# Optimization experiments

Hardware: AMD Instinct MI355X
Metric: run time of the kernel (lower is better)

Reference implementation:

```python
import jax, jax.numpy as jnp
import numpy as np

B, T, D = 1, 1024, 1024
H, KVH, HD = 16, 4, 64          # heads, kv heads, head dim (D = H*HD)
E, K, FF = 8, 2, 2048           # experts, top_k, expert hidden
CF, ROPE_THETA, CLIP = 2.0, 500000.0, 8.0
CAP = int(np.ceil(B * T * K * CF / E))  # per-expert capacity (=512)
EPS = 1e-5


def layernorm(x, w):
    mu = jnp.mean(x, -1, keepdims=True)
    var = jnp.var(x, -1, keepdims=True)
    return (x - mu) * jax.lax.rsqrt(var + EPS) * w


def rotate_half(u):
    u1, u2 = u[..., : HD // 2], u[..., HD // 2 :]
    return jnp.concatenate([-u2, u1], axis=-1)


def rope(q, k, position_ids):
    inv_freq = 1.0 / (ROPE_THETA ** (jnp.arange(0, HD, 2, dtype=jnp.float32) / HD))
    ang = position_ids.astype(jnp.float32)[..., None] * inv_freq  # (B,T,HD/2)
    emb = jnp.concatenate([ang, ang], axis=-1)                    # (B,T,HD)
    cos = jnp.cos(emb)[:, :, None, :]  # broadcast over heads -> (B,T,1,HD)
    sin = jnp.sin(emb)[:, :, None, :]
    q = q * cos + rotate_half(q) * sin
    k = k * cos + rotate_half(k) * sin
    return q, k


def setup_inputs() -> dict:
    key = jax.random.key(0)
    ks = jax.random.split(key, 12)
    s = 0.02
    return {
        "hidden_states": jax.random.normal(ks[0], (B, T, D), jnp.float32),
        "position_ids": jnp.tile(jnp.arange(T, dtype=jnp.int32)[None, :], (B, 1)),
        "ln1_w": jnp.ones((D,), jnp.float32),
        "ln2_w": jnp.ones((D,), jnp.float32),
        "Wq": jax.random.normal(ks[1], (D, H * HD), jnp.float32) * s,
        "Wk": jax.random.normal(ks[2], (D, KVH * HD), jnp.float32) * s,
        "Wv": jax.random.normal(ks[3], (D, KVH * HD), jnp.float32) * s,
        "Wo": jax.random.normal(ks[4], (H * HD, D), jnp.float32) * s,
        "Wr": jax.random.normal(ks[5], (D, E), jnp.float32) * s,
        "Wg": jax.random.normal(ks[6], (E, D, FF), jnp.float32) * s,
        "Wu": jax.random.normal(ks[7], (E, D, FF), jnp.float32) * s,
        "Wd": jax.random.normal(ks[8], (E, FF, D), jnp.float32) * s,
    }


def reference(hidden_states, position_ids, ln1_w, ln2_w, Wq, Wk, Wv, Wo, Wr, Wg, Wu, Wd):
    x = hidden_states
    # ---- attention (pre-LN, clip_qkv, RoPE, GQA, causal) ----
    res = x
    h = layernorm(x, ln1_w)
    q = jnp.clip(h @ Wq, -CLIP, CLIP).reshape(B, T, H, HD)
    k = jnp.clip(h @ Wk, -CLIP, CLIP).reshape(B, T, KVH, HD)
    v = jnp.clip(h @ Wv, -CLIP, CLIP).reshape(B, T, KVH, HD)
    q, k = rope(q, k, position_ids)
    k = jnp.repeat(k, H // KVH, axis=2)  # GQA expand -> (B,T,H,HD)
    v = jnp.repeat(v, H // KVH, axis=2)
    scores = jnp.einsum("bthd,bshd->bhts", q, k) / jnp.sqrt(jnp.float32(HD))
    causal = jnp.tril(jnp.ones((T, T), bool))
    scores = jnp.where(causal[None, None], scores, jnp.finfo(scores.dtype).min)
    attn = jax.nn.softmax(scores, axis=-1)
    o = jnp.einsum("bhts,bshd->bthd", attn, v).reshape(B, T, H * HD) @ Wo
    x = res + o
    # ---- MoE FFN (top-k router, capacity-based dispatch, GLU experts) ----
    res = x
    h = layernorm(x, ln2_w).reshape(B * T, D)
    N = B * T
    probs = jax.nn.softmax(h @ Wr, axis=-1)            # (N,E)
    vals, idx = jax.lax.top_k(probs, K)                # (N,K)
    gate = vals / jnp.sum(vals, -1, keepdims=True)     # normalize_top_k_affinities
    e_flat = idx.reshape(-1)                           # (N*K,)
    g_flat = gate.reshape(-1)
    tok = jnp.repeat(jnp.arange(N), K)                 # source token per assignment
    oh = jax.nn.one_hot(e_flat, E, dtype=jnp.int32)
    pos = jnp.cumsum(oh, axis=0)[jnp.arange(N * K), e_flat] - 1  # slot within expert
    keep = pos < CAP                                   # capacity drop mask
    slot = jnp.where(keep, pos, CAP)                   # overflow -> trash slot
    xb = jnp.zeros((E, CAP + 1, D), h.dtype).at[e_flat, slot].set(h[tok])
    act = jax.nn.silu(jnp.einsum("ecd,edf->ecf", xb, Wg)) * jnp.einsum("ecd,edf->ecf", xb, Wu)
    ob = jnp.einsum("ecf,efd->ecd", act, Wd)           # (E,CAP+1,D)
    contrib = ob[e_flat, slot] * (g_flat * keep.astype(h.dtype))[:, None]
    y = jnp.zeros((N, D), h.dtype).at[tok].add(contrib).reshape(B, T, D)
    return res + y
```

## Files before the change

### kernel.cpp

```cpp
#include <hip/hip_runtime.h>
#include <math.h>

typedef __attribute__((ext_vector_type(8))) short bfrag;
typedef __attribute__((ext_vector_type(8))) unsigned short u16x8;
typedef __attribute__((ext_vector_type(4))) float f32x4;

__device__ __forceinline__ unsigned short bf16_rne(float f) {
  unsigned int u = __float_as_uint(f);
  u += 0x7FFFu + ((u >> 16) & 1u);
  return (unsigned short)(u >> 16);
}
__device__ __forceinline__ float bf16f(unsigned short h) {
  return __uint_as_float(((unsigned int)h) << 16);
}
__device__ __forceinline__ void split3(float x, unsigned short &o1, unsigned short &o2, unsigned short &o3) {
  o1 = bf16_rne(x);
  const float r1 = x - bf16f(o1);
  o2 = bf16_rne(r1);
  const float r2 = r1 - bf16f(o2);
  o3 = bf16_rne(r2);
}
__device__ __forceinline__ void split2(float x, unsigned short &o1, unsigned short &o2) {
  o1 = bf16_rne(x);
  o2 = bf16_rne(x - bf16f(o1));
}

__global__ __launch_bounds__(256) void ln_kernel(const float* __restrict__ x,
                                                 const float* __restrict__ w,
                                                 float* __restrict__ out) {
  const int t = blockIdx.x;
  const int tid = threadIdx.x;
  const float4 v = *reinterpret_cast<const float4*>(&x[(size_t)t * 1024 + tid * 4]);
  float s = v.x + v.y + v.z + v.w;
  float ss = v.x * v.x + v.y * v.y + v.z * v.z + v.w * v.w;
#pragma unroll
  for (int off = 32; off; off >>= 1) {
    s += __shfl_xor(s, off);
    ss += __shfl_xor(ss, off);
  }
  __shared__ float red1[4], red2[4];
  if ((tid & 63) == 0) { red1[tid >> 6] = s; red2[tid >> 6] = ss; }
  __syncthreads();
  s = red1[0] + red1[1] + red1[2] + red1[3];
  ss = red2[0] + red2[1] + red2[2] + red2[3];
  const float mu = s * (1.0f / 1024.0f);
  const float var = ss * (1.0f / 1024.0f) - mu * mu;
  const float rstd = 1.0f / sqrtf(var + 1e-5f);
  const float4 wv = *reinterpret_cast<const float4*>(&w[tid * 4]);
  float4 o;
  o.x = (v.x - mu) * rstd * wv.x;
  o.y = (v.y - mu) * rstd * wv.y;
  o.z = (v.z - mu) * rstd * wv.z;
  o.w = (v.w - mu) * rstd * wv.w;
  *reinterpret_cast<float4*>(&out[(size_t)t * 1024 + tid * 4]) = o;
}

__global__ __launch_bounds__(256) void split3_conv_kernel(
    const float* __restrict__ src, unsigned short* __restrict__ d1,
    unsigned short* __restrict__ d2, unsigned short* __restrict__ d3) {
  const int i = blockIdx.x * 256 + threadIdx.x;
  const float4 v = reinterpret_cast<const float4*>(src)[i];
  ushort4 a, b, c;
  split3(v.x, a.x, b.x, c.x);
  split3(v.y, a.y, b.y, c.y);
  split3(v.z, a.z, b.z, c.z);
  split3(v.w, a.w, b.w, c.w);
  reinterpret_cast<ushort4*>(d1)[i] = a;
  reinterpret_cast<ushort4*>(d2)[i] = b;
  reinterpret_cast<ushort4*>(d3)[i] = c;
}

__global__ __launch_bounds__(256) void split3t_kernel(
    const float* __restrict__ src, unsigned short* __restrict__ d1,
    unsigned short* __restrict__ d2, unsigned short* __restrict__ d3,
    int K, int N) {
  __shared__ float tile[32][33];
  const int k0 = blockIdx.x * 32, n0 = blockIdx.y * 32;
  const int tx = threadIdx.x & 31, ty = threadIdx.x >> 5;
#pragma unroll
  for (int i = 0; i < 4; ++i)
    tile[ty + i * 8][tx] = src[(size_t)(k0 + ty + i * 8) * N + n0 + tx];
  __syncthreads();
#pragma unroll
  for (int i = 0; i < 4; ++i) {
    const float v = tile[tx][ty + i * 8];
    unsigned short s1, s2, s3;
    split3(v, s1, s2, s3);
    const size_t o = (size_t)(n0 + ty + i * 8) * K + k0 + tx;
    d1[o] = s1; d2[o] = s2; d3[o] = s3;
  }
}

__global__ __launch_bounds__(256) void gemm_ps_kernel(
    const unsigned short* __restrict__ A1, const unsigned short* __restrict__ A2,
    const unsigned short* __restrict__ A3, const unsigned short* __restrict__ B1,
    const unsigned short* __restrict__ B2, const unsigned short* __restrict__ B3,
    float* __restrict__ C, const float* __restrict__ Res,
    int N, int K, int doclip) {
  __shared__ alignas(16) unsigned short As[3][32][40];
  __shared__ alignas(16) unsigned short Bs[3][64][40];
  const int tid = threadIdx.x;
  const int m0 = blockIdx.x * 32;
  const int n0 = blockIdx.y * 64;
  const int w = tid >> 6, l = tid & 63;
  const int wm = (w & 1) * 16, wn = (w >> 1) * 32;
  const int lr = l & 15, lg = l >> 4;
  const int arow = tid >> 3, aslot = tid & 7;

  const unsigned short* Ap[3] = {A1, A2, A3};
  const unsigned short* Bp[3] = {B1, B2, B3};

  f32x4 acc[2] = {{0.f,0.f,0.f,0.f},{0.f,0.f,0.f,0.f}};

  for (int k0 = 0; k0 < K; k0 += 32) {
#pragma unroll
    for (int s = 0; s < 3; ++s) {
      *reinterpret_cast<ushort4*>(&As[s][arow][aslot * 4]) =
          *reinterpret_cast<const ushort4*>(&Ap[s][(size_t)(m0 + arow) * K + k0 + aslot * 4]);
#pragma unroll
      for (int p = 0; p < 2; ++p) {
        const int row = arow + p * 32;
        *reinterpret_cast<ushort4*>(&Bs[s][row][aslot * 4]) =
            *reinterpret_cast<const ushort4*>(&Bp[s][(size_t)(n0 + row) * K + k0 + aslot * 4]);
      }
    }
    __syncthreads();
    bfrag af[3], bg[2][3];
#pragma unroll
    for (int s = 0; s < 3; ++s)
      af[s] = *reinterpret_cast<const bfrag*>(&As[s][wm + lr][lg * 8]);
#pragma unroll
    for (int ni = 0; ni < 2; ++ni)
#pragma unroll
      for (int s = 0; s < 3; ++s)
        bg[ni][s] = *reinterpret_cast<const bfrag*>(&Bs[s][wn + ni * 16 + lr][lg * 8]);
#pragma unroll
    for (int ni = 0; ni < 2; ++ni) {
      f32x4 c = acc[ni];
      c = __builtin_amdgcn_mfma_f32_16x16x32_bf16(af[2], bg[ni][0], c, 0, 0, 0);
      c = __builtin_amdgcn_mfma_f32_16x16x32_bf16(af[1], bg[ni][1], c, 0, 0, 0);
      c = __builtin_amdgcn_mfma_f32_16x16x32_bf16(af[0], bg[ni][2], c, 0, 0, 0);
      c = __builtin_amdgcn_mfma_f32_16x16x32_bf16(af[1], bg[ni][0], c, 0, 0, 0);
      c = __builtin_amdgcn_mfma_f32_16x16x32_bf16(af[0], bg[ni][1], c, 0, 0, 0);
      c = __builtin_amdgcn_mfma_f32_16x16x32_bf16(af[0], bg[ni][0], c, 0, 0, 0);
      acc[ni] = c;
    }
    __syncthreads();
  }
#pragma unroll
  for (int ni = 0; ni < 2; ++ni)
#pragma unroll
    for (int r = 0; r < 4; ++r) {
      const int row = m0 + wm + lg * 4 + r;
      const int col = n0 + wn + ni * 16 + lr;
      float vv = acc[ni][r];
      if (doclip) vv = fminf(fmaxf(vv, -8.0f), 8.0f);
      if (Res) vv += Res[(size_t)row * N + col];
      C[(size_t)row * N + col] = vv;
    }
}

__global__ void rope_table_kernel(const int* __restrict__ posids,
                                  float* __restrict__ cosT, float* __restrict__ sinT) {
  const int t = blockIdx.x * 8 + (threadIdx.x >> 5);
  const int i = threadIdx.x & 31;
  const double ang = (double)posids[t] * pow(500000.0, -(double)i / 32.0);
  cosT[t * 32 + i] = (float)cos(ang);
  sinT[t * 32 + i] = (float)sin(ang);
}

__global__ void rope_kernel(float* __restrict__ q, float* __restrict__ k,
                            const float* __restrict__ cosT, const float* __restrict__ sinT) {
  const int t = blockIdx.x;
  const int hh = blockIdx.y;
  const int i = threadIdx.x;
  float* ptr = (hh < 16) ? &q[((size_t)t * 16 + hh) * 64]
                         : &k[((size_t)t * 4 + (hh - 16)) * 64];
  const float c = cosT[t * 32 + i], s = sinT[t * 32 + i];
  const float u1 = ptr[i], u2 = ptr[i + 32];
  ptr[i]      = u1 * c - u2 * s;
  ptr[i + 32] = u2 * c + u1 * s;
}

__global__ __launch_bounds__(256) void prep_kv_kernel(
    const float* __restrict__ k, const float* __restrict__ v,
    unsigned short* __restrict__ Kp1, unsigned short* __restrict__ Kp2,
    unsigned short* __restrict__ Vp1, unsigned short* __restrict__ Vp2) {
  const int key = blockIdx.x;
  const int kvh = threadIdx.x >> 6;
  const int d = threadIdx.x & 63;
  const float kk = k[((size_t)key * 4 + kvh) * 64 + d];
  const float vv = v[((size_t)key * 4 + kvh) * 64 + d];
  unsigned short a1, a2, b1, b2;
  split2(kk, a1, a2);
  split2(vv, b1, b2);
  const size_t ki = ((size_t)kvh * 1024 + key) * 64 + d;
  Kp1[ki] = a1; Kp2[ki] = a2;
  const size_t vi = ((size_t)kvh * 64 + d) * 1024 + key;
  Vp1[vi] = b1; Vp2[vi] = b2;
}

__global__ __launch_bounds__(256) void attn_kernel(
    const float* __restrict__ q,
    const unsigned short* __restrict__ Kp1, const unsigned short* __restrict__ Kp2,
    const unsigned short* __restrict__ Vp1, const unsigned short* __restrict__ Vp2,
    float* __restrict__ o) {
  const int qt = blockIdx.x, h = blockIdx.y, kvh = h >> 2;
  __shared__ unsigned short Ks1[64][72], Ks2[64][72], Vt1[64][72], Vt2[64][72];
  __shared__ unsigned short Ps1[4][16][72], Ps2[4][16][72];
  const int tid = threadIdx.x;
  const int w = tid >> 6, l = tid & 63;
  const int lr = l & 15, lg = l >> 4;

  bfrag aq1[2], aq2[2];
  {
    const int tq = qt * 64 + w * 16 + lr;
    const float* qrow = &q[((size_t)tq * 16 + h) * 64];
#pragma unroll
    for (int ks = 0; ks < 2; ++ks) {
      const int d0 = ks * 32 + lg * 8;
      const float4 f0 = *reinterpret_cast<const float4*>(qrow + d0);
      const float4 f1 = *reinterpret_cast<const float4*>(qrow + d0 + 4);
      const float xv[8] = {f0.x, f0.y, f0.z, f0.w, f1.x, f1.y, f1.z, f1.w};
#pragma unroll
      for (int j = 0; j < 8; ++j) {
        const float xs = xv[j] * 0.125f;
        unsigned short p1, p2;
        split2(xs, p1, p2);
        aq1[ks][j] = (short)p1;
        aq2[ks][j] = (short)p2;
      }
    }
  }

  f32x4 accO[4] = {{0.f,0.f,0.f,0.f},{0.f,0.f,0.f,0.f},{0.f,0.f,0.f,0.f},{0.f,0.f,0.f,0.f}};
  float mrun[4] = {-INFINITY, -INFINITY, -INFINITY, -INFINITY};
  float lrun[4] = {0.f, 0.f, 0.f, 0.f};

  for (int ti = 0; ti <= qt; ++ti) {
    const int s0 = ti * 64;
    {
      const size_t kbase = ((size_t)kvh * 1024 + s0 + l) * 64 + w * 16;
      *reinterpret_cast<u16x8*>(&Ks1[l][w * 16])     = *reinterpret_cast<const u16x8*>(&Kp1[kbase]);
      *reinterpret_cast<u16x8*>(&Ks1[l][w * 16 + 8]) = *reinterpret_cast<const u16x8*>(&Kp1[kbase + 8]);
      *reinterpret_cast<u16x8*>(&Ks2[l][w * 16])     = *reinterpret_cast<const u16x8*>(&Kp2[kbase]);
      *reinterpret_cast<u16x8*>(&Ks2[l][w * 16 + 8]) = *reinterpret_cast<const u16x8*>(&Kp2[kbase + 8]);
      const size_t vbase = ((size_t)kvh * 64 + l) * 1024 + s0 + w * 16;
      *reinterpret_cast<u16x8*>(&Vt1[l][w * 16])     = *reinterpret_cast<const u16x8*>(&Vp1[vbase]);
      *reinterpret_cast<u16x8*>(&Vt1[l][w * 16 + 8]) = *reinterpret_cast<const u16x8*>(&Vp1[vbase + 8]);
      *reinterpret_cast<u16x8*>(&Vt2[l][w * 16])     = *reinterpret_cast<const u16x8*>(&Vp2[vbase]);
      *reinterpret_cast<u16x8*>(&Vt2[l][w * 16 + 8]) = *reinterpret_cast<const u16x8*>(&Vp2[vbase + 8]);
    }
    __syncthreads();

    f32x4 accS[4] = {{0.f,0.f,0.f,0.f},{0.f,0.f,0.f,0.f},{0.f,0.f,0.f,0.f},{0.f,0.f,0.f,0.f}};
#pragma unroll
    for (int ks = 0; ks < 2; ++ks) {
      const int koff = ks * 32 + lg * 8;
#pragma unroll
      for (int ni = 0; ni < 4; ++ni) {
        const bfrag b1 = *reinterpret_cast<const bfrag*>(&Ks1[ni * 16 + lr][koff]);
        const bfrag b2 = *reinterpret_cast<const bfrag*>(&Ks2[ni * 16 + lr][koff]);
        f32x4 c = accS[ni];
        c = __builtin_amdgcn_mfma_f32_16x16x32_bf16(aq1[ks], b2, c, 0, 0, 0);
        c = __builtin_amdgcn_mfma_f32_16x16x32_bf16(aq2[ks], b1, c, 0, 0, 0);
        c = __builtin_amdgcn_mfma_f32_16x16x32_bf16(aq1[ks], b1, c, 0, 0, 0);
        accS[ni] = c;
      }
    }
    if (ti == qt) {
      const int rowb = w * 16 + lg * 4;
#pragma unroll
      for (int ni = 0; ni < 4; ++ni)
#pragma unroll
        for (int r = 0; r < 4; ++r)
          if (ni * 16 + lr > rowb + r) accS[ni][r] = -INFINITY;
    }
    float alpha[4];
#pragma unroll
    for (int r = 0; r < 4; ++r) {
      float tm = fmaxf(fmaxf(accS[0][r], accS[1][r]), fmaxf(accS[2][r], accS[3][r]));
      tm = fmaxf(tm, __shfl_xor(tm, 1));
      tm = fmaxf(tm, __shfl_xor(tm, 2));
      tm = fmaxf(tm, __shfl_xor(tm, 4));
      tm = fmaxf(tm, __shfl_xor(tm, 8));
      const float mnew = fmaxf(mrun[r], tm);
      alpha[r] = __expf(mrun[r] - mnew);
      mrun[r] = mnew;
      float ps = 0.f;
#pragma unroll
      for (int ni = 0; ni < 4; ++ni) {
        const float pv = __expf(accS[ni][r] - mnew);
        accS[ni][r] = pv;
        ps += pv;
      }
      ps += __shfl_xor(ps, 1);
      ps += __shfl_xor(ps, 2);
      ps += __shfl_xor(ps, 4);
      ps += __shfl_xor(ps, 8);
      lrun[r] = lrun[r] * alpha[r] + ps;
    }
#pragma unroll
    for (int ni = 0; ni < 4; ++ni)
#pragma unroll
      for (int r = 0; r < 4; ++r) {
        const float pv = accS[ni][r];
        unsigned short p1, p2;
        split2(pv, p1, p2);
        Ps1[w][lg * 4 + r][ni * 16 + lr] = p1;
        Ps2[w][lg * 4 + r][ni * 16 + lr] = p2;
      }
#pragma unroll
    for (int ni = 0; ni < 4; ++ni)
#pragma unroll
      for (int r = 0; r < 4; ++r) accO[ni][r] *= alpha[r];

    asm volatile("s_waitcnt lgkmcnt(0)" ::: "memory");

#pragma unroll
    for (int kk = 0; kk < 2; ++kk) {
      const int koff = kk * 32 + lg * 8;
      const bfrag pa1 = *reinterpret_cast<const bfrag*>(&Ps1[w][lr][koff]);
      const bfrag pa2 = *reinterpret_cast<const bfrag*>(&Ps2[w][lr][koff]);
#pragma unroll
      for (int ni = 0; ni < 4; ++ni) {
        const bfrag vb1 = *reinterpret_cast<const bfrag*>(&Vt1[ni * 16 + lr][koff]);
        const bfrag vb2 = *reinterpret_cast<const bfrag*>(&Vt2[ni * 16 + lr][koff]);
        f32x4 c = accO[ni];
        c = __builtin_amdgcn_mfma_f32_16x16x32_bf16(pa1, vb2, c, 0, 0, 0);
        c = __builtin_amdgcn_mfma_f32_16x16x32_bf16(pa2, vb1, c, 0, 0, 0);
        c = __builtin_amdgcn_mfma_f32_16x16x32_bf16(pa1, vb1, c, 0, 0, 0);
        accO[ni] = c;
      }
    }
    __syncthreads();
  }

  const int tqo = qt * 64 + w * 16 + lg * 4;
#pragma unroll
  for (int r = 0; r < 4; ++r) {
    const float inv = 1.0f / lrun[r];
#pragma unroll
    for (int ni = 0; ni < 4; ++ni)
      o[((size_t)(tqo + r) * 16 + h) * 64 + ni * 16 + lr] = accO[ni][r] * inv;
  }
}

__global__ __launch_bounds__(64) void router_kernel(const float* __restrict__ h2,
                                                    const float* __restrict__ Wr,
                                                    int* __restrict__ eidx,
                                                    float* __restrict__ egate) {
  const int t = blockIdx.x;
  const int l = threadIdx.x;
  float p[8];
#pragma unroll
  for (int e = 0; e < 8; ++e) p[e] = 0.f;
  for (int d = l; d < 1024; d += 64) {
    const float x = h2[(size_t)t * 1024 + d];
    const float4 w0 = *reinterpret_cast<const float4*>(&Wr[d * 8]);
    const float4 w1 = *reinterpret_cast<const float4*>(&Wr[d * 8 + 4]);
    p[0] += x * w0.x; p[1] += x * w0.y; p[2] += x * w0.z; p[3] += x * w0.w;
    p[4] += x * w1.x; p[5] += x * w1.y; p[6] += x * w1.z; p[7] += x * w1.w;
  }
#pragma unroll
  for (int off = 32; off; off >>= 1) {
#pragma unroll
    for (int e = 0; e < 8; ++e) p[e] += __shfl_xor(p[e], off);
  }
  if (l == 0) {
    int i0 = 0; float b0 = p[0];
#pragma unroll
    for (int e = 1; e < 8; ++e) if (p[e] > b0) { b0 = p[e]; i0 = e; }
    int i1 = -1; float b1 = -INFINITY;
#pragma unroll
    for (int e = 0; e < 8; ++e) if (e != i0 && p[e] > b1) { b1 = p[e]; i1 = e; }
    const float ex = expf(b1 - b0);
    eidx[t * 2] = i0; eidx[t * 2 + 1] = i1;
    egate[t * 2] = 1.0f / (1.0f + ex);
    egate[t * 2 + 1] = ex / (1.0f + ex);
  }
}

__global__ __launch_bounds__(256) void dispatch_kernel(
    const int* __restrict__ eidx, int* __restrict__ cnt,
    int* __restrict__ slot_token, int* __restrict__ entry_slot) {
  __shared__ unsigned char ef[2048];
  __shared__ unsigned short ch[256][8];
  const int tid = threadIdx.x;
  for (int i = tid; i < 2048; i += 256) ef[i] = (unsigned char)eidx[i];
  __syncthreads();
  int loc[8];
#pragma unroll
  for (int e = 0; e < 8; ++e) loc[e] = 0;
  const int base = tid * 8;
  for (int j = 0; j < 8; ++j) {
    const int ee = ef[base + j];
#pragma unroll
    for (int e = 0; e < 8; ++e) loc[e] += (ee == e);
  }
#pragma unroll
  for (int e = 0; e < 8; ++e) ch[tid][e] = (unsigned short)loc[e];
  __syncthreads();
  int pre[8];
#pragma unroll
  for (int e = 0; e < 8; ++e) pre[e] = 0;
  for (int t2 = 0; t2 < tid; ++t2) {
#pragma unroll
    for (int e = 0; e < 8; ++e) pre[e] += ch[t2][e];
  }
  if (tid == 255) {
#pragma unroll
    for (int e = 0; e < 8; ++e) cnt[e] = min(pre[e] + loc[e], 512);
  }
  for (int j = 0; j < 8; ++j) {
    const int i = base + j;
    const int ee = ef[i];
    int slot = 0;
#pragma unroll
    for (int e = 0; e < 8; ++e) {
      if (e == ee) { slot = pre[e]; pre[e] = pre[e] + 1; }
    }
    if (slot < 512) {
      slot_token[ee * 512 + slot] = i >> 1;
      entry_slot[i] = slot;
    } else {
      entry_slot[i] = -1;
    }
  }
}

__global__ __launch_bounds__(256) void moe_xbf_kernel(
    const float* __restrict__ h2, const int* __restrict__ cnt,
    const int* __restrict__ slot_token, unsigned short* __restrict__ xbf) {
  const int row = blockIdx.x;
  const int e = row >> 9, slot = row & 511;
  const int tid = threadIdx.x;
  ushort4 o;
  if (slot < cnt[e]) {
    const int tok = slot_token[row];
    const float4 f = *reinterpret_cast<const float4*>(&h2[(size_t)tok * 1024 + tid * 4]);
    o = make_ushort4(bf16_rne(f.x), bf16_rne(f.y), bf16_rne(f.z), bf16_rne(f.w));
  } else {
    o = make_ushort4(0, 0, 0, 0);
  }
  *reinterpret_cast<ushort4*>(&xbf[(size_t)row * 1024 + tid * 4]) = o;
}

__global__ __launch_bounds__(256, 2) void moe_mlp1_kernel(
    const unsigned short* __restrict__ xbf, const float* __restrict__ Wg,
    const float* __restrict__ Wu, const int* __restrict__ cnt,
    unsigned short* __restrict__ act) {
  const int bx = blockIdx.x;
  const int e = bx & 7, nt = bx >> 3;
  const int n0 = nt * 32;
  const int ce = cnt[e];
  if (ce <= 0) return;
  __shared__ alignas(16) unsigned short BgL[2][32][72], BuL[2][32][72];
  const int tid = threadIdx.x;
  const int w = tid >> 6, l = tid & 63;
  const int lr = l & 15, lg = l >> 4;
  const int wc = tid & 31, kq8 = tid >> 5;
  const float* WgE = Wg + (size_t)e * 1024 * 2048 + (size_t)kq8 * 8 * 2048 + n0 + wc;
  const float* WuE = Wu + (size_t)e * 1024 * 2048 + (size_t)kq8 * 8 * 2048 + n0 + wc;
  const unsigned short* xbE = xbf + (size_t)e * 512 * 1024;

  f32x4 accG[8][2], accU[8][2];
#pragma unroll
  for (int mi = 0; mi < 8; ++mi)
#pragma unroll
    for (int ni = 0; ni < 2; ++ni) {
      accG[mi][ni] = (f32x4){0.f, 0.f, 0.f, 0.f};
      accU[mi][ni] = (f32x4){0.f, 0.f, 0.f, 0.f};
    }

  float wgr[8], wur[8];
#pragma unroll
  for (int j = 0; j < 8; ++j) { wgr[j] = WgE[(size_t)j * 2048]; wur[j] = WuE[(size_t)j * 2048]; }
  {
    u16x8 g8, u8;
#pragma unroll
    for (int j = 0; j < 8; ++j) { g8[j] = bf16_rne(wgr[j]); u8[j] = bf16_rne(wur[j]); }
    *reinterpret_cast<u16x8*>(&BgL[0][wc][kq8 * 8]) = g8;
    *reinterpret_cast<u16x8*>(&BuL[0][wc][kq8 * 8]) = u8;
  }
#pragma unroll
  for (int j = 0; j < 8; ++j) { wgr[j] = WgE[(size_t)(64 + j) * 2048]; wur[j] = WuE[(size_t)(64 + j) * 2048]; }
  __syncthreads();

  for (int t = 0; t < 16; ++t) {
    const int cur = t & 1;
    bfrag bgf[2][2], buf2[2][2];
#pragma unroll
    for (int ni = 0; ni < 2; ++ni)
#pragma unroll
      for (int kf = 0; kf < 2; ++kf) {
        bgf[ni][kf]  = *reinterpret_cast<const bfrag*>(&BgL[cur][ni * 16 + lr][kf * 32 + lg * 8]);
        buf2[ni][kf] = *reinterpret_cast<const bfrag*>(&BuL[cur][ni * 16 + lr][kf * 32 + lg * 8]);
      }
    u16x8 g8, u8;
    if (t < 15) {
#pragma unroll
      for (int j = 0; j < 8; ++j) { g8[j] = bf16_rne(wgr[j]); u8[j] = bf16_rne(wur[j]); }
    }
    if (t < 14) {
      const size_t kb = (size_t)(t + 2) * 64;
#pragma unroll
      for (int j = 0; j < 8; ++j) { wgr[j] = WgE[(kb + j) * 2048]; wur[j] = WuE[(kb + j) * 2048]; }
    }
    const int kA = t * 64 + lg * 8;
#pragma unroll
    for (int mi = 0; mi < 8; ++mi) {
      const int row0 = (mi * 4 + w) * 16;
      if (row0 < ce) {
        const unsigned short* ap = &xbE[(size_t)(row0 + lr) * 1024 + kA];
        const bfrag a0 = *reinterpret_cast<const bfrag*>(ap);
        const bfrag a1 = *reinterpret_cast<const bfrag*>(ap + 32);
#pragma unroll
        for (int ni = 0; ni < 2; ++ni) {
          accG[mi][ni] = __builtin_amdgcn_mfma_f32_16x16x32_bf16(a0, bgf[ni][0], accG[mi][ni], 0, 0, 0);
          accG[mi][ni] = __builtin_amdgcn_mfma_f32_16x16x32_bf16(a1, bgf[ni][1], accG[mi][ni], 0, 0, 0);
          accU[mi][ni] = __builtin_amdgcn_mfma_f32_16x16x32_bf16(a0, buf2[ni][0], accU[mi][ni], 0, 0, 0);
          accU[mi][ni] = __builtin_amdgcn_mfma_f32_16x16x32_bf16(a1, buf2[ni][1], accU[mi][ni], 0, 0, 0);
        }
      }
    }
    if (t < 15) {
      *reinterpret_cast<u16x8*>(&BgL[cur ^ 1][wc][kq8 * 8]) = g8;
      *reinterpret_cast<u16x8*>(&BuL[cur ^ 1][wc][kq8 * 8]) = u8;
    }
    __syncthreads();
  }
#pragma unroll
  for (int mi = 0; mi < 8; ++mi) {
    const int row0 = (mi * 4 + w) * 16;
    if (row0 < ce) {
#pragma unroll
      for (int r = 0; r < 4; ++r) {
        const int m = row0 + lg * 4 + r;
        if (m < ce) {
#pragma unroll
          for (int ni = 0; ni < 2; ++ni) {
            const float gg = accG[mi][ni][r];
            const float uu = accU[mi][ni][r];
            const float a = gg / (1.0f + __expf(-gg)) * uu;
            act[((size_t)e * 512 + m) * 2048 + n0 + ni * 16 + lr] = bf16_rne(a);
          }
        }
      }
    }
  }
}

__global__ __launch_bounds__(256, 2) void moe_mlp2_kernel(
    const unsigned short* __restrict__ act, const float* __restrict__ Wd,
    const int* __restrict__ cnt, float* __restrict__ ob) {
  const int bx = blockIdx.x;
  const int e = bx & 7;
  const int rr = bx >> 3;
  const int nt = rr & 31, kc = rr >> 5;
  const int n0 = nt * 32;
  const int ce = cnt[e];
  if (ce <= 0) return;
  __shared__ alignas(16) unsigned short BsL[2][32][72];
  const int tid = threadIdx.x;
  const int w = tid >> 6, l = tid & 63;
  const int lr = l & 15, lg = l >> 4;
  const int wc = tid & 31, kq8 = tid >> 5;
  const unsigned short* actE = act + (size_t)e * 512 * 2048 + (size_t)kc * 1024;
  const float* WdE = Wd + (size_t)e * 2048 * 1024 + (size_t)(kc * 1024 + kq8 * 8) * 1024 + n0 + wc;
  float* obE = ob + (size_t)kc * 8 * 512 * 1024;

  f32x4 acc[8][2];
#pragma unroll
  for (int mi = 0; mi < 8; ++mi)
#pragma unroll
    for (int ni = 0; ni < 2; ++ni) acc[mi][ni] = (f32x4){0.f, 0.f, 0.f, 0.f};

  float wdr[8];
#pragma unroll
  for (int j = 0; j < 8; ++j) wdr[j] = WdE[(size_t)j * 1024];
  {
    u16x8 d8;
#pragma unroll
    for (int j = 0; j < 8; ++j) d8[j] = bf16_rne(wdr[j]);
    *reinterpret_cast<u16x8*>(&BsL[0][wc][kq8 * 8]) = d8;
  }
#pragma unroll
  for (int j = 0; j < 8; ++j) wdr[j] = WdE[(size_t)(64 + j) * 1024];
  __syncthreads();

  for (int t = 0; t < 16; ++t) {
    const int cur = t & 1;
    bfrag bf2[2][2];
#pragma unroll
    for (int ni = 0; ni < 2; ++ni)
#pragma unroll
      for (int kf = 0; kf < 2; ++kf)
        bf2[ni][kf] = *reinterpret_cast<const bfrag*>(&BsL[cur][ni * 16 + lr][kf * 32 + lg * 8]);
    u16x8 d8;
    if (t < 15) {
#pragma unroll
      for (int j = 0; j < 8; ++j) d8[j] = bf16_rne(wdr[j]);
    }
    if (t < 14) {
      const size_t kb = (size_t)(t + 2) * 64;
#pragma unroll
      for (int j = 0; j < 8; ++j) wdr[j] = WdE[(kb + j) * 1024];
    }
    const int kA = t * 64 + lg * 8;
#pragma unroll
    for (int mi = 0; mi < 8; ++mi) {
      const int row0 = (mi * 4 + w) * 16;
      if (row0 < ce) {
        const unsigned short* ap = &actE[(size_t)(row0 + lr) * 2048 + kA];
        const bfrag a0 = *reinterpret_cast<const bfrag*>(ap);
        const bfrag a1 = *reinterpret_cast<const bfrag*>(ap + 32);
#pragma unroll
        for (int ni = 0; ni < 2; ++ni) {
          acc[mi][ni] = __builtin_amdgcn_mfma_f32_16x16x32_bf16(a0, bf2[ni][0], acc[mi][ni], 0, 0, 0);
          acc[mi][ni] = __builtin_amdgcn_mfma_f32_16x16x32_bf16(a1, bf2[ni][1], acc[mi][ni], 0, 0, 0);
        }
      }
    }
    if (t < 15) {
      *reinterpret_cast<u16x8*>(&BsL[cur ^ 1][wc][kq8 * 8]) = d8;
    }
    __syncthreads();
  }
#pragma unroll
  for (int mi = 0; mi < 8; ++mi) {
    const int row0 = (mi * 4 + w) * 16;
    if (row0 < ce) {
#pragma unroll
      for (int r = 0; r < 4; ++r) {
        const int m = row0 + lg * 4 + r;
        if (m < ce) {
#pragma unroll
          for (int ni = 0; ni < 2; ++ni)
            obE[((size_t)e * 512 + m) * 1024 + n0 + ni * 16 + lr] = acc[mi][ni][r];
        }
      }
    }
  }
}

__global__ __launch_bounds__(256) void combine_kernel(
    const float* __restrict__ ob, const int* __restrict__ eidx,
    const float* __restrict__ egate, const int* __restrict__ entry_slot,
    float* __restrict__ out) {
  const int t = blockIdx.x;
  const int d = threadIdx.x * 4;
  const size_t half = (size_t)8 * 512 * 1024;
  float4 o4 = *reinterpret_cast<float4*>(&out[(size_t)t * 1024 + d]);
#pragma unroll
  for (int kk = 0; kk < 2; ++kk) {
    const int i = t * 2 + kk;
    const int s = entry_slot[i];
    if (s >= 0) {
      const int e = eidx[i];
      const float g = egate[i];
      const size_t base = ((size_t)e * 512 + s) * 1024 + d;
      const float4 c0 = *reinterpret_cast<const float4*>(&ob[base]);
      const float4 c1 = *reinterpret_cast<const float4*>(&ob[half + base]);
      o4.x += g * (c0.x + c1.x); o4.y += g * (c0.y + c1.y);
      o4.z += g * (c0.z + c1.z); o4.w += g * (c0.w + c1.w);
    }
  }
  *reinterpret_cast<float4*>(&out[(size_t)t * 1024 + d]) = o4;
}

extern "C" void kernel_launch(void* const* d_in, const int* in_sizes, int n_in,
                              void* d_out, int out_size, void* d_ws, size_t ws_size,
                              hipStream_t stream) {
  const float* hidden = (const float*)d_in[0];
  const int* posids  = (const int*)d_in[1];
  const float* ln1w  = (const float*)d_in[2];
  const float* ln2w  = (const float*)d_in[3];
  const float* Wq    = (const float*)d_in[4];
  const float* Wk    = (const float*)d_in[5];
  const float* Wv    = (const float*)d_in[6];
  const float* Wo    = (const float*)d_in[7];
  const float* Wr    = (const float*)d_in[8];
  const float* Wg    = (const float*)d_in[9];
  const float* Wu    = (const float*)d_in[10];
  const float* Wd    = (const float*)d_in[11];
  float* out = (float*)d_out;

  char* p = (char*)d_ws;
  auto alloc = [&](size_t bytes) { char* r = p; p += (bytes + 255) & ~(size_t)255; return r; };
  float* h1   = (float*)alloc((size_t)1024 * 1024 * 4);
  float* qb   = (float*)alloc((size_t)1024 * 1024 * 4);
  float* kb   = (float*)alloc((size_t)1024 * 256 * 4);
  float* vb   = (float*)alloc((size_t)1024 * 256 * 4);
  float* ao   = (float*)alloc((size_t)1024 * 1024 * 4);
  float* h2   = (float*)alloc((size_t)1024 * 1024 * 4);
  unsigned short* act = (unsigned short*)alloc((size_t)8 * 512 * 2048 * 2);
  float* obuf = (float*)alloc((size_t)2 * 8 * 512 * 1024 * 4);
  int* eidx   = (int*)alloc(2048 * 4);
  float* egate = (float*)alloc(2048 * 4);
  int* cnt    = (int*)alloc(8 * 4);
  int* slot_token = (int*)alloc((size_t)8 * 512 * 4);
  int* entry_slot = (int*)alloc(2048 * 4);
  float* cosT = (float*)alloc((size_t)1024 * 32 * 4);
  float* sinT = (float*)alloc((size_t)1024 * 32 * 4);
  unsigned short* Kp1 = (unsigned short*)alloc((size_t)4 * 1024 * 64 * 2);
  unsigned short* Kp2 = (unsigned short*)alloc((size_t)4 * 1024 * 64 * 2);
  unsigned short* Vp1 = (unsigned short*)alloc((size_t)4 * 1024 * 64 * 2);
  unsigned short* Vp2 = (unsigned short*)alloc((size_t)4 * 1024 * 64 * 2);
  unsigned short* xbf = (unsigned short*)alloc((size_t)8 * 512 * 1024 * 2);
  const size_t MK = (size_t)1024 * 1024;
  unsigned short* h1s[3], *aos[3], *wqt[3], *wkt[3], *wvt[3], *wot[3];
  for (int s = 0; s < 3; ++s) h1s[s] = (unsigned short*)alloc(MK * 2);
  for (int s = 0; s < 3; ++s) aos[s] = (unsigned short*)alloc(MK * 2);
  for (int s = 0; s < 3; ++s) wqt[s] = (unsigned short*)alloc(MK * 2);
  for (int s = 0; s < 3; ++s) wkt[s] = (unsigned short*)alloc((size_t)256 * 1024 * 2);
  for (int s = 0; s < 3; ++s) wvt[s] = (unsigned short*)alloc((size_t)256 * 1024 * 2);
  for (int s = 0; s < 3; ++s) wot[s] = (unsigned short*)alloc(MK * 2);

  rope_table_kernel<<<128, 256, 0, stream>>>(posids, cosT, sinT);
  split3t_kernel<<<dim3(32, 32), 256, 0, stream>>>(Wq, wqt[0], wqt[1], wqt[2], 1024, 1024);
  split3t_kernel<<<dim3(32, 8),  256, 0, stream>>>(Wk, wkt[0], wkt[1], wkt[2], 1024, 256);
  split3t_kernel<<<dim3(32, 8),  256, 0, stream>>>(Wv, wvt[0], wvt[1], wvt[2], 1024, 256);
  split3t_kernel<<<dim3(32, 32), 256, 0, stream>>>(Wo, wot[0], wot[1], wot[2], 1024, 1024);

  ln_kernel<<<1024, 256, 0, stream>>>(hidden, ln1w, h1);
  split3_conv_kernel<<<1024, 256, 0, stream>>>(h1, h1s[0], h1s[1], h1s[2]);
  gemm_ps_kernel<<<dim3(32, 16), 256, 0, stream>>>(h1s[0], h1s[1], h1s[2],
      wqt[0], wqt[1], wqt[2], qb, nullptr, 1024, 1024, 1);
  gemm_ps_kernel<<<dim3(32, 4), 256, 0, stream>>>(h1s[0], h1s[1], h1s[2],
      wkt[0], wkt[1], wkt[2], kb, nullptr, 256, 1024, 1);
  gemm_ps_kernel<<<dim3(32, 4), 256, 0, stream>>>(h1s[0], h1s[1], h1s[2],
      wvt[0], wvt[1], wvt[2], vb, nullptr, 256, 1024, 1);
  rope_kernel<<<dim3(1024, 20), 32, 0, stream>>>(qb, kb, cosT, sinT);
  prep_kv_kernel<<<1024, 256, 0, stream>>>(kb, vb, Kp1, Kp2, Vp1, Vp2);
  attn_kernel<<<dim3(16, 16), 256, 0, stream>>>(qb, Kp1, Kp2, Vp1, Vp2, ao);
  split3_conv_kernel<<<1024, 256, 0, stream>>>(ao, aos[0], aos[1], aos[2]);
  gemm_ps_kernel<<<dim3(32, 16), 256, 0, stream>>>(aos[0], aos[1], aos[2],
      wot[0], wot[1], wot[2], out, hidden, 1024, 1024, 0);
  ln_kernel<<<1024, 256, 0, stream>>>(out, ln2w, h2);
  router_kernel<<<1024, 64, 0, stream>>>(h2, Wr, eidx, egate);
  dispatch_kernel<<<1, 256, 0, stream>>>(eidx, cnt, slot_token, entry_slot);
  moe_xbf_kernel<<<4096, 256, 0, stream>>>(h2, cnt, slot_token, xbf);
  moe_mlp1_kernel<<<512, 256, 0, stream>>>(xbf, Wg, Wu, cnt, act);
  moe_mlp2_kernel<<<512, 256, 0, stream>>>(act, Wd, cnt, obuf);
  combine_kernel<<<1024, 256, 0, stream>>>(obuf, eidx, egate, entry_slot, out);
}
```

Measured before the change: 361.2 us.

## Fuse layernorm with bf16 split, merge QKV GEMMs, split attention output in-kernel

Folds the first layernorm into the three-way bf16 split so the fp32 normalized activations are never written and reread. Merges the three separate Q, K and V projection GEMM launches into one grid of 24 column-block rows that picks its weights by block index. The attention kernel now writes its output directly as three bf16 split planes, so the separate conversion kernel and its fp32 buffer are gone. This removes three launches and two fp32 round trips through memory, at the cost of extra register and ALU work in the attention epilogue.

```diff
diff --git a/kernel.cpp b/kernel.cpp
--- a/kernel.cpp
+++ b/kernel.cpp
@@ -55,16 +55,40 @@
   *reinterpret_cast<float4*>(&out[(size_t)t * 1024 + tid * 4]) = o;
 }
 
-__global__ __launch_bounds__(256) void split3_conv_kernel(
-    const float* __restrict__ src, unsigned short* __restrict__ d1,
-    unsigned short* __restrict__ d2, unsigned short* __restrict__ d3) {
-  const int i = blockIdx.x * 256 + threadIdx.x;
-  const float4 v = reinterpret_cast<const float4*>(src)[i];
+__global__ __launch_bounds__(256) void ln_split3_kernel(
+    const float* __restrict__ x, const float* __restrict__ w,
+    unsigned short* __restrict__ d1, unsigned short* __restrict__ d2,
+    unsigned short* __restrict__ d3) {
+  const int t = blockIdx.x;
+  const int tid = threadIdx.x;
+  const float4 v = *reinterpret_cast<const float4*>(&x[(size_t)t * 1024 + tid * 4]);
+  float s = v.x + v.y + v.z + v.w;
+  float ss = v.x * v.x + v.y * v.y + v.z * v.z + v.w * v.w;
+#pragma unroll
+  for (int off = 32; off; off >>= 1) {
+    s += __shfl_xor(s, off);
+    ss += __shfl_xor(ss, off);
+  }
+  __shared__ float red1[4], red2[4];
+  if ((tid & 63) == 0) { red1[tid >> 6] = s; red2[tid >> 6] = ss; }
+  __syncthreads();
+  s = red1[0] + red1[1] + red1[2] + red1[3];
+  ss = red2[0] + red2[1] + red2[2] + red2[3];
+  const float mu = s * (1.0f / 1024.0f);
+  const float var = ss * (1.0f / 1024.0f) - mu * mu;
+  const float rstd = 1.0f / sqrtf(var + 1e-5f);
+  const float4 wv = *reinterpret_cast<const float4*>(&w[tid * 4]);
+  float4 o;
+  o.x = (v.x - mu) * rstd * wv.x;
+  o.y = (v.y - mu) * rstd * wv.y;
+  o.z = (v.z - mu) * rstd * wv.z;
+  o.w = (v.w - mu) * rstd * wv.w;
   ushort4 a, b, c;
-  split3(v.x, a.x, b.x, c.x);
-  split3(v.y, a.y, b.y, c.y);
-  split3(v.z, a.z, b.z, c.z);
-  split3(v.w, a.w, b.w, c.w);
+  split3(o.x, a.x, b.x, c.x);
+  split3(o.y, a.y, b.y, c.y);
+  split3(o.z, a.z, b.z, c.z);
+  split3(o.w, a.w, b.w, c.w);
+  const int i = t * 256 + tid;
   reinterpret_cast<ushort4*>(d1)[i] = a;
   reinterpret_cast<ushort4*>(d2)[i] = b;
   reinterpret_cast<ushort4*>(d3)[i] = c;
@@ -91,17 +115,15 @@
   }
 }
 
-__global__ __launch_bounds__(256) void gemm_ps_kernel(
+__device__ __forceinline__ void gemm_ps_body(
     const unsigned short* __restrict__ A1, const unsigned short* __restrict__ A2,
     const unsigned short* __restrict__ A3, const unsigned short* __restrict__ B1,
     const unsigned short* __restrict__ B2, const unsigned short* __restrict__ B3,
     float* __restrict__ C, const float* __restrict__ Res,
-    int N, int K, int doclip) {
+    int N, int K, int doclip, int m0, int n0) {
   __shared__ alignas(16) unsigned short As[3][32][40];
   __shared__ alignas(16) unsigned short Bs[3][64][40];
   const int tid = threadIdx.x;
-  const int m0 = blockIdx.x * 32;
-  const int n0 = blockIdx.y * 64;
   const int w = tid >> 6, l = tid & 63;
   const int wm = (w & 1) * 16, wn = (w >> 1) * 32;
   const int lr = l & 15, lg = l >> 4;
@@ -158,6 +180,36 @@
       if (Res) vv += Res[(size_t)row * N + col];
       C[(size_t)row * N + col] = vv;
     }
+}
+
+__global__ __launch_bounds__(256) void gemm_ps_kernel(
+    const unsigned short* __restrict__ A1, const unsigned short* __restrict__ A2,
+    const unsigned short* __restrict__ A3, const unsigned short* __restrict__ B1,
+    const unsigned short* __restrict__ B2, const unsigned short* __restrict__ B3,
+    float* __restrict__ C, const float* __restrict__ Res,
+    int N, int K, int doclip) {
+  gemm_ps_body(A1, A2, A3, B1, B2, B3, C, Res, N, K, doclip,
+               blockIdx.x * 32, blockIdx.y * 64);
+}
+
+__global__ __launch_bounds__(256) void gemm_qkv_kernel(
+    const unsigned short* __restrict__ A1, const unsigned short* __restrict__ A2,
+    const unsigned short* __restrict__ A3,
+    const unsigned short* __restrict__ Q1, const unsigned short* __restrict__ Q2,
+    const unsigned short* __restrict__ Q3,
+    const unsigned short* __restrict__ K1, const unsigned short* __restrict__ K2,
+    const unsigned short* __restrict__ K3,
+    const unsigned short* __restrict__ V1, const unsigned short* __restrict__ V2,
+    const unsigned short* __restrict__ V3,
+    float* __restrict__ qb, float* __restrict__ kb, float* __restrict__ vb) {
+  const int by = blockIdx.y;
+  const unsigned short *B1, *B2, *B3;
+  float* C;
+  int N, n0;
+  if (by < 16)      { B1 = Q1; B2 = Q2; B3 = Q3; C = qb; N = 1024; n0 = by * 64; }
+  else if (by < 20) { B1 = K1; B2 = K2; B3 = K3; C = kb; N = 256;  n0 = (by - 16) * 64; }
+  else              { B1 = V1; B2 = V2; B3 = V3; C = vb; N = 256;  n0 = (by - 20) * 64; }
+  gemm_ps_body(A1, A2, A3, B1, B2, B3, C, nullptr, N, 1024, 1, blockIdx.x * 32, n0);
 }
 
 __global__ void rope_table_kernel(const int* __restrict__ posids,
@@ -204,7 +256,8 @@
     const float* __restrict__ q,
     const unsigned short* __restrict__ Kp1, const unsigned short* __restrict__ Kp2,
     const unsigned short* __restrict__ Vp1, const unsigned short* __restrict__ Vp2,
-    float* __restrict__ o) {
+    unsigned short* __restrict__ o1, unsigned short* __restrict__ o2,
+    unsigned short* __restrict__ o3) {
   const int qt = blockIdx.x, h = blockIdx.y, kvh = h >> 2;
   __shared__ unsigned short Ks1[64][72], Ks2[64][72], Vt1[64][72], Vt2[64][72];
   __shared__ unsigned short Ps1[4][16][72], Ps2[4][16][72];
@@ -341,8 +394,12 @@
   for (int r = 0; r < 4; ++r) {
     const float inv = 1.0f / lrun[r];
 #pragma unroll
-    for (int ni = 0; ni < 4; ++ni)
-      o[((size_t)(tqo + r) * 16 + h) * 64 + ni * 16 + lr] = accO[ni][r] * inv;
+    for (int ni = 0; ni < 4; ++ni) {
+      const size_t oi = (size_t)(tqo + r) * 1024 + h * 64 + ni * 16 + lr;
+      unsigned short s1, s2, s3;
+      split3(accO[ni][r] * inv, s1, s2, s3);
+      o1[oi] = s1; o2[oi] = s2; o3[oi] = s3;
+    }
   }
 }
 
@@ -688,11 +745,9 @@
 
   char* p = (char*)d_ws;
   auto alloc = [&](size_t bytes) { char* r = p; p += (bytes + 255) & ~(size_t)255; return r; };
-  float* h1   = (float*)alloc((size_t)1024 * 1024 * 4);
   float* qb   = (float*)alloc((size_t)1024 * 1024 * 4);
   float* kb   = (float*)alloc((size_t)1024 * 256 * 4);
   float* vb   = (float*)alloc((size_t)1024 * 256 * 4);
-  float* ao   = (float*)alloc((size_t)1024 * 1024 * 4);
   float* h2   = (float*)alloc((size_t)1024 * 1024 * 4);
   unsigned short* act = (unsigned short*)alloc((size_t)8 * 512 * 2048 * 2);
   float* obuf = (float*)alloc((size_t)2 * 8 * 512 * 1024 * 4);
@@ -723,18 +778,14 @@
   split3t_kernel<<<dim3(32, 8),  256, 0, stream>>>(Wv, wvt[0], wvt[1], wvt[2], 1024, 256);
   split3t_kernel<<<dim3(32, 32), 256, 0, stream>>>(Wo, wot[0], wot[1], wot[2], 1024, 1024);
 
-  ln_kernel<<<1024, 256, 0, stream>>>(hidden, ln1w, h1);
-  split3_conv_kernel<<<1024, 256, 0, stream>>>(h1, h1s[0], h1s[1], h1s[2]);
-  gemm_ps_kernel<<<dim3(32, 16), 256, 0, stream>>>(h1s[0], h1s[1], h1s[2],
-      wqt[0], wqt[1], wqt[2], qb, nullptr, 1024, 1024, 1);
-  gemm_ps_kernel<<<dim3(32, 4), 256, 0, stream>>>(h1s[0], h1s[1], h1s[2],
-      wkt[0], wkt[1], wkt[2], kb, nullptr, 256, 1024, 1);
-  gemm_ps_kernel<<<dim3(32, 4), 256, 0, stream>>>(h1s[0], h1s[1], h1s[2],
-      wvt[0], wvt[1], wvt[2], vb, nullptr, 256, 1024, 1);
+  ln_split3_kernel<<<1024, 256, 0, stream>>>(hidden, ln1w, h1s[0], h1s[1], h1s[2]);
+  gemm_qkv_kernel<<<dim3(32, 24), 256, 0, stream>>>(h1s[0], h1s[1], h1s[2],
+      wqt[0], wqt[1], wqt[2], wkt[0], wkt[1], wkt[2], wvt[0], wvt[1], wvt[2],
+      qb, kb, vb);
   rope_kernel<<<dim3(1024, 20), 32, 0, stream>>>(qb, kb, cosT, sinT);
   prep_kv_kernel<<<1024, 256, 0, stream>>>(kb, vb, Kp1, Kp2, Vp1, Vp2);
-  attn_kernel<<<dim3(16, 16), 256, 0, stream>>>(qb, Kp1, Kp2, Vp1, Vp2, ao);
-  split3_conv_kernel<<<1024, 256, 0, stream>>>(ao, aos[0], aos[1], aos[2]);
+  attn_kernel<<<dim3(16, 16), 256, 0, stream>>>(qb, Kp1, Kp2, Vp1, Vp2,
+      aos[0], aos[1], aos[2]);
   gemm_ps_kernel<<<dim3(32, 16), 256, 0, stream>>>(aos[0], aos[1], aos[2],
       wot[0], wot[1], wot[2], out, hidden, 1024, 1024, 0);
   ln_kernel<<<1024, 256, 0, stream>>>(out, ln2w, h2);
```

New measurement: 312.0 us. -13.6%, faster.
